# Kernel tuning notes

Hardware: AMD Instinct MI355X
Metric: run time of the kernel (lower is better)

Reference implementation:

```python
import jax, jax.numpy as jnp
import numpy as np


def setup_inputs() -> dict:
    key = jax.random.key(0)
    k1, k2, k3 = jax.random.split(key, 3)
    Lq, Lkv, H, D = 2048, 2048, 16, 128
    return {
        "query": jax.random.normal(k1, (Lq, H, D), dtype=jnp.float32),
        "key": jax.random.normal(k2, (Lkv, H, D), dtype=jnp.float32),
        "value": jax.random.normal(k3, (Lkv, H, D), dtype=jnp.float32),
    }


def reference(query, key, value):
    # query: [Lq, H, D], key: [Lkv, H, D], value: [Lkv, H, Dv]
    # Original module performs chunked online-softmax attention; the math is
    # exactly scaled-dot-product softmax attention with scale 1/sqrt(k_features).
    d = query.shape[-1]
    q = query * (1.0 / jnp.sqrt(jnp.asarray(d, dtype=query.dtype)))
    scores = jnp.einsum('qhd,khd->qhk', q, key)          # [Lq, H, Lkv]
    weights = jax.nn.softmax(scores, axis=-1)            # numerically stable online softmax equivalent
    out = jnp.einsum('qhk,khf->qhf', weights, value)     # [Lq, H, Dv]
    return out
```

## Files before the change

### kernel.cpp

```cpp
#include <hip/hip_runtime.h>
#include <hip/hip_bf16.h>

typedef __bf16 bf16x8 __attribute__((ext_vector_type(8)));
typedef __bf16 bf16x4 __attribute__((ext_vector_type(4)));
typedef __bf16 bf16x2 __attribute__((ext_vector_type(2)));
typedef float  f32x16 __attribute__((ext_vector_type(16)));
typedef float  f32x4  __attribute__((ext_vector_type(4)));

#define HD     2048
#define DH     128
#define KVT    64
#define NCH    16
#define NSPLIT 2
#define NROWS  32768
#define VSTR   68

__device__ __forceinline__ int kkey_of(int r) {
    return r & 7;
}

__global__ __launch_bounds__(512, 2)
void fmha_kern(const float* __restrict__ Qg, const float* __restrict__ Kg,
               const float* __restrict__ Vg, __bf16* __restrict__ wsOb,
               float* __restrict__ wsML)
{
    __shared__ __align__(16) __bf16 klds[2][KVT * 128];
    __shared__ __align__(16) __bf16 vtlds[2][DH * VSTR];

    const int tid  = threadIdx.x;
    const int lane = tid & 63;
    const int wrp  = tid >> 6;
    const int g    = lane >> 5;
    const int l31  = lane & 31;

    const int b    = blockIdx.x;
    const int grp  = b & 31;
    const int qblk = b >> 5;
    const int h    = grp >> 1;
    const int sp   = grp & 1;
    const int t0   = sp * NCH;

    const float qscale = 1.4426950408889634f * 0.08838834764831845f;
    const int q = qblk * 256 + wrp * 32 + l31;

    bf16x8 qf[8];
    {
        const float* qrow = Qg + (size_t)q * HD + h * DH;
        #pragma unroll
        for (int j = 0; j < 8; ++j) {
            f32x4 a = *(const f32x4*)(qrow + j * 16 + 8 * g);
            f32x4 c = *(const f32x4*)(qrow + j * 16 + 8 * g + 4);
            bf16x8 f;
            f[0] = (__bf16)(a[0] * qscale); f[1] = (__bf16)(a[1] * qscale);
            f[2] = (__bf16)(a[2] * qscale); f[3] = (__bf16)(a[3] * qscale);
            f[4] = (__bf16)(c[0] * qscale); f[5] = (__bf16)(c[1] * qscale);
            f[6] = (__bf16)(c[2] * qscale); f[7] = (__bf16)(c[3] * qscale);
            qf[j] = f;
        }
    }

    const int krow = tid >> 3, kc = tid & 7;
    const int kvp  = tid & 31, vdv0 = (tid >> 5) * 8;
    const float* kbase = Kg + (size_t)h * DH;
    const float* vbase = Vg + (size_t)h * DH;

    f32x4 kreg0, kreg1, kreg2, kreg3, vreg0, vreg1, vreg2, vreg3;

    auto stage_load = [&](int t) {
        const float* kp = kbase + (size_t)(t * KVT + krow) * HD + kc * 16;
        kreg0 = *(const f32x4*)(kp);
        kreg1 = *(const f32x4*)(kp + 4);
        kreg2 = *(const f32x4*)(kp + 8);
        kreg3 = *(const f32x4*)(kp + 12);
        const float* vp = vbase + (size_t)(t * KVT + 2 * kvp) * HD + vdv0;
        vreg0 = *(const f32x4*)(vp);
        vreg1 = *(const f32x4*)(vp + 4);
        vreg2 = *(const f32x4*)(vp + HD);
        vreg3 = *(const f32x4*)(vp + HD + 4);
    };

    auto stage_write = [&](int buf) {
        bf16x8 k0, k1;
        k0[0]=(__bf16)kreg0[0]; k0[1]=(__bf16)kreg0[1]; k0[2]=(__bf16)kreg0[2]; k0[3]=(__bf16)kreg0[3];
        k0[4]=(__bf16)kreg1[0]; k0[5]=(__bf16)kreg1[1]; k0[6]=(__bf16)kreg1[2]; k0[7]=(__bf16)kreg1[3];
        k1[0]=(__bf16)kreg2[0]; k1[1]=(__bf16)kreg2[1]; k1[2]=(__bf16)kreg2[2]; k1[3]=(__bf16)kreg2[3];
        k1[4]=(__bf16)kreg3[0]; k1[5]=(__bf16)kreg3[1]; k1[6]=(__bf16)kreg3[2]; k1[7]=(__bf16)kreg3[3];
        const int key = kkey_of(krow);
        *(bf16x8*)&klds[buf][krow * 128 + (((kc * 2)     ^ key) << 3)] = k0;
        *(bf16x8*)&klds[buf][krow * 128 + (((kc * 2 + 1) ^ key) << 3)] = k1;
        #pragma unroll
        for (int e = 0; e < 8; ++e) {
            bf16x2 w;
            w[0] = (__bf16)((e < 4) ? vreg0[e & 3] : vreg1[e & 3]);
            w[1] = (__bf16)((e < 4) ? vreg2[e & 3] : vreg3[e & 3]);
            *(bf16x2*)&vtlds[buf][(vdv0 + e) * VSTR + 2 * kvp] = w;
        }
    };

    auto block_sync = []() {
        asm volatile("s_waitcnt lgkmcnt(0)" ::: "memory");
        __builtin_amdgcn_s_barrier();
    };

    float mrun = -1e30f, lrun = 0.0f;
    f32x16 o0, o1, o2, o3;
    #pragma unroll
    for (int r = 0; r < 16; ++r) { o0[r] = 0.f; o1[r] = 0.f; o2[r] = 0.f; o3[r] = 0.f; }

    stage_load(t0);
    stage_write(0);
    stage_load(t0 + 1);
    block_sync();

    const int kkey = kkey_of(l31);

    #pragma unroll 2
    for (int tt = 0; tt < NCH; ++tt) {
        const int cur = tt & 1;

        f32x16 s0, s1;
        #pragma unroll
        for (int r = 0; r < 16; ++r) { s0[r] = 0.f; s1[r] = 0.f; }
        __builtin_amdgcn_s_setprio(1);
        #pragma unroll
        for (int j = 0; j < 8; ++j) {
            const int gcol = ((2 * j + g) ^ kkey) << 3;
            bf16x8 kf0 = *(const bf16x8*)&klds[cur][l31 * 128 + gcol];
            s0 = __builtin_amdgcn_mfma_f32_32x32x16_bf16(kf0, qf[j], s0, 0, 0, 0);
            bf16x8 kf1 = *(const bf16x8*)&klds[cur][(32 + l31) * 128 + gcol];
            s1 = __builtin_amdgcn_mfma_f32_32x32x16_bf16(kf1, qf[j], s1, 0, 0, 0);
        }
        __builtin_amdgcn_s_setprio(0);

        if (tt + 1 < NCH) stage_write(cur ^ 1);
        if (tt + 2 < NCH) stage_load(t0 + tt + 2);

        float m16[8];
        #pragma unroll
        for (int r = 0; r < 8; ++r)
            m16[r] = fmaxf(fmaxf(s0[r], s0[r + 8]), fmaxf(s1[r], s1[r + 8]));
        float tmax = fmaxf(fmaxf(fmaxf(m16[0], m16[4]), fmaxf(m16[1], m16[5])),
                           fmaxf(fmaxf(m16[2], m16[6]), fmaxf(m16[3], m16[7])));
        tmax = fmaxf(tmax, __shfl_xor(tmax, 32, 64));

        if (__any(tmax > mrun + 8.0f)) {
            const float mnew  = fmaxf(mrun, tmax);
            const float alpha = __builtin_amdgcn_exp2f(mrun - mnew);
            lrun *= alpha;
            #pragma unroll
            for (int r = 0; r < 16; ++r) { o0[r]*=alpha; o1[r]*=alpha; o2[r]*=alpha; o3[r]*=alpha; }
            mrun = mnew;
        }

        #pragma unroll
        for (int r = 0; r < 16; ++r) {
            s0[r] = __builtin_amdgcn_exp2f(s0[r] - mrun);
            s1[r] = __builtin_amdgcn_exp2f(s1[r] - mrun);
        }
        float ps = 0.f;
        #pragma unroll
        for (int r = 0; r < 16; ++r) ps += s0[r] + s1[r];
        lrun += ps;

        bf16x8 pfa0, pfa1, pfb0, pfb1;
        #pragma unroll
        for (int e = 0; e < 8; ++e) {
            pfa0[e] = (__bf16)s0[e]; pfa1[e] = (__bf16)s0[8 + e];
            pfb0[e] = (__bf16)s1[e]; pfb1[e] = (__bf16)s1[8 + e];
        }

        __builtin_amdgcn_s_setprio(1);
        #pragma unroll
        for (int bb = 0; bb < 4; ++bb) {
            const __bf16* vb = &vtlds[cur][(bb * 32 + l31) * VSTR];
            f32x16& oo = (bb == 0) ? o0 : (bb == 1) ? o1 : (bb == 2) ? o2 : o3;
            bf16x8 va;
            bf16x4 a0, a1;
            a0 = *(const bf16x4*)(vb + 4 * g);
            a1 = *(const bf16x4*)(vb + 8 + 4 * g);
            va[0]=a0[0]; va[1]=a0[1]; va[2]=a0[2]; va[3]=a0[3];
            va[4]=a1[0]; va[5]=a1[1]; va[6]=a1[2]; va[7]=a1[3];
            oo = __builtin_amdgcn_mfma_f32_32x32x16_bf16(va, pfa0, oo, 0, 0, 0);
            a0 = *(const bf16x4*)(vb + 16 + 4 * g);
            a1 = *(const bf16x4*)(vb + 24 + 4 * g);
            va[0]=a0[0]; va[1]=a0[1]; va[2]=a0[2]; va[3]=a0[3];
            va[4]=a1[0]; va[5]=a1[1]; va[6]=a1[2]; va[7]=a1[3];
            oo = __builtin_amdgcn_mfma_f32_32x32x16_bf16(va, pfa1, oo, 0, 0, 0);
            a0 = *(const bf16x4*)(vb + 32 + 4 * g);
            a1 = *(const bf16x4*)(vb + 40 + 4 * g);
            va[0]=a0[0]; va[1]=a0[1]; va[2]=a0[2]; va[3]=a0[3];
            va[4]=a1[0]; va[5]=a1[1]; va[6]=a1[2]; va[7]=a1[3];
            oo = __builtin_amdgcn_mfma_f32_32x32x16_bf16(va, pfb0, oo, 0, 0, 0);
            a0 = *(const bf16x4*)(vb + 48 + 4 * g);
            a1 = *(const bf16x4*)(vb + 56 + 4 * g);
            va[0]=a0[0]; va[1]=a0[1]; va[2]=a0[2]; va[3]=a0[3];
            va[4]=a1[0]; va[5]=a1[1]; va[6]=a1[2]; va[7]=a1[3];
            oo = __builtin_amdgcn_mfma_f32_32x32x16_bf16(va, pfb1, oo, 0, 0, 0);
        }
        __builtin_amdgcn_s_setprio(0);

        if (tt + 1 < NCH) block_sync();
    }

    const float ltot  = lrun + __shfl_xor(lrun, 32, 64);
    const int   rowid = q * 16 + h;

    __bf16* orow = wsOb + ((size_t)sp * NROWS + rowid) * 128;
    #pragma unroll
    for (int bb = 0; bb < 4; ++bb) {
        const f32x16& oo = (bb == 0) ? o0 : (bb == 1) ? o1 : (bb == 2) ? o2 : o3;
        #pragma unroll
        for (int jj = 0; jj < 4; ++jj) {
            bf16x4 v;
            v[0] = (__bf16)oo[4*jj+0]; v[1] = (__bf16)oo[4*jj+1];
            v[2] = (__bf16)oo[4*jj+2]; v[3] = (__bf16)oo[4*jj+3];
            *(bf16x4*)(orow + bb * 32 + 8 * jj + 4 * g) = v;
        }
    }
    if (lane < 32) {
        float* ml = wsML + ((size_t)sp * NROWS + rowid) * 2;
        ml[0] = mrun;
        ml[1] = ltot;
    }
}

__global__ __launch_bounds__(256, 4)
void fmha_combine(const __bf16* __restrict__ wsOb, const float* __restrict__ wsML,
                  float* __restrict__ Og)
{
    const int tid   = threadIdx.x;
    const int rowid = blockIdx.x * 8 + (tid >> 5);
    const int c     = (tid & 31) * 4;

    float m[NSPLIT], l[NSPLIT];
    float M = -1e30f;
    #pragma unroll
    for (int s = 0; s < NSPLIT; ++s) {
        const float* ml = wsML + ((size_t)s * NROWS + rowid) * 2;
        m[s] = ml[0]; l[s] = ml[1];
        M = fmaxf(M, m[s]);
    }
    float L = 0.f, w[NSPLIT];
    #pragma unroll
    for (int s = 0; s < NSPLIT; ++s) {
        w[s] = __builtin_amdgcn_exp2f(m[s] - M);
        L += l[s] * w[s];
    }
    const float inv = 1.0f / L;

    f32x4 acc; acc[0]=0.f; acc[1]=0.f; acc[2]=0.f; acc[3]=0.f;
    #pragma unroll
    for (int s = 0; s < NSPLIT; ++s) {
        bf16x4 v = *(const bf16x4*)(wsOb + ((size_t)s * NROWS + rowid) * 128 + c);
        acc[0] += (float)v[0] * w[s]; acc[1] += (float)v[1] * w[s];
        acc[2] += (float)v[2] * w[s]; acc[3] += (float)v[3] * w[s];
    }
    f32x4 r;
    r[0] = acc[0]*inv; r[1] = acc[1]*inv; r[2] = acc[2]*inv; r[3] = acc[3]*inv;
    *(f32x4*)(Og + (size_t)rowid * 128 + c) = r;
}

__global__ __launch_bounds__(256, 2)
void fmha_fb(const float* __restrict__ Qg, const float* __restrict__ Kg,
             const float* __restrict__ Vg, float* __restrict__ Og)
{
    __shared__ __align__(16) __bf16 klds[2][32 * 128];
    __shared__ __align__(16) __bf16 vtlds[2][DH * 36];

    const int tid  = threadIdx.x;
    const int lane = tid & 63;
    const int wrp  = tid >> 6;
    const int g    = lane >> 5;
    const int l31  = lane & 31;

    const int b    = blockIdx.x;
    const int h    = 2 * (b & 7) + ((b >> 3) >> 4);
    const int qblk = (b >> 3) & 15;

    const float qscale = 1.4426950408889634f * 0.08838834764831845f;
    const int q = qblk * 128 + wrp * 32 + l31;

    bf16x8 qf[8];
    {
        const float* qrow = Qg + (size_t)q * HD + h * DH;
        #pragma unroll
        for (int db = 0; db < 8; ++db) {
            f32x4 a = *(const f32x4*)(qrow + db * 16 + 8 * g);
            f32x4 c = *(const f32x4*)(qrow + db * 16 + 8 * g + 4);
            bf16x8 f;
            f[0] = (__bf16)(a[0] * qscale); f[1] = (__bf16)(a[1] * qscale);
            f[2] = (__bf16)(a[2] * qscale); f[3] = (__bf16)(a[3] * qscale);
            f[4] = (__bf16)(c[0] * qscale); f[5] = (__bf16)(c[1] * qscale);
            f[6] = (__bf16)(c[2] * qscale); f[7] = (__bf16)(c[3] * qscale);
            qf[db] = f;
        }
    }

    const int krow = tid >> 3, kc = tid & 7;
    const int vkv  = tid & 31, vdv0 = (tid >> 5) * 16;
    const float* kbase = Kg + (size_t)h * DH;
    const float* vbase = Vg + (size_t)h * DH;

    f32x4 kreg0, kreg1, kreg2, kreg3, vreg0, vreg1, vreg2, vreg3;

    auto stage_load = [&](int t) {
        const float* kp = kbase + (size_t)(t * 32 + krow) * HD + kc * 8;
        kreg0 = *(const f32x4*)(kp);
        kreg1 = *(const f32x4*)(kp + 4);
        kreg2 = *(const f32x4*)(kp + 64);
        kreg3 = *(const f32x4*)(kp + 68);
        const float* vp = vbase + (size_t)(t * 32 + vkv) * HD + vdv0;
        vreg0 = *(const f32x4*)(vp);
        vreg1 = *(const f32x4*)(vp + 4);
        vreg2 = *(const f32x4*)(vp + 8);
        vreg3 = *(const f32x4*)(vp + 12);
    };

    auto stage_write = [&](int buf) {
        bf16x8 k0, k1;
        k0[0]=(__bf16)kreg0[0]; k0[1]=(__bf16)kreg0[1]; k0[2]=(__bf16)kreg0[2]; k0[3]=(__bf16)kreg0[3];
        k0[4]=(__bf16)kreg1[0]; k0[5]=(__bf16)kreg1[1]; k0[6]=(__bf16)kreg1[2]; k0[7]=(__bf16)kreg1[3];
        k1[0]=(__bf16)kreg2[0]; k1[1]=(__bf16)kreg2[1]; k1[2]=(__bf16)kreg2[2]; k1[3]=(__bf16)kreg2[3];
        k1[4]=(__bf16)kreg3[0]; k1[5]=(__bf16)kreg3[1]; k1[6]=(__bf16)kreg3[2]; k1[7]=(__bf16)kreg3[3];
        const int swz = (krow & 7) << 3;
        *(bf16x8*)&klds[buf][krow * 128 + ((kc * 8) ^ swz)]      = k0;
        *(bf16x8*)&klds[buf][krow * 128 + ((kc * 8 + 64) ^ swz)] = k1;
        #pragma unroll
        for (int jj = 0; jj < 4; ++jj) {
            f32x4 vv = (jj == 0) ? vreg0 : (jj == 1) ? vreg1 : (jj == 2) ? vreg2 : vreg3;
            #pragma unroll
            for (int e = 0; e < 4; ++e)
                vtlds[buf][(vdv0 + jj * 4 + e) * 36 + vkv] = (__bf16)vv[e];
        }
    };

    float mrun = -1e30f, lrun = 0.0f;
    f32x16 o0, o1, o2, o3;
    #pragma unroll
    for (int r = 0; r < 16; ++r) { o0[r] = 0.f; o1[r] = 0.f; o2[r] = 0.f; o3[r] = 0.f; }

    stage_load(0);
    stage_write(0);

    for (int tt = 0; tt < 64; ++tt) {
        const int cur = tt & 1;
        if (tt + 1 < 64) stage_load(tt + 1);
        __syncthreads();

        f32x16 sa, sb;
        #pragma unroll
        for (int r = 0; r < 16; ++r) { sa[r] = 0.f; sb[r] = 0.f; }
        const int kswz = (l31 & 7) << 3;
        #pragma unroll
        for (int db = 0; db < 4; ++db) {
            bf16x8 kfa = *(const bf16x8*)&klds[cur][l31 * 128 + (((2*db)   * 16 + g * 8) ^ kswz)];
            sa = __builtin_amdgcn_mfma_f32_32x32x16_bf16(kfa, qf[2*db],   sa, 0, 0, 0);
            bf16x8 kfb = *(const bf16x8*)&klds[cur][l31 * 128 + (((2*db+1) * 16 + g * 8) ^ kswz)];
            sb = __builtin_amdgcn_mfma_f32_32x32x16_bf16(kfb, qf[2*db+1], sb, 0, 0, 0);
        }
        f32x16 s;
        #pragma unroll
        for (int r = 0; r < 16; ++r) s[r] = sa[r] + sb[r];

        float m8[8];
        #pragma unroll
        for (int r = 0; r < 8; ++r) m8[r] = fmaxf(s[r], s[r + 8]);
        float tmax = fmaxf(fmaxf(fmaxf(m8[0], m8[4]), fmaxf(m8[1], m8[5])),
                           fmaxf(fmaxf(m8[2], m8[6]), fmaxf(m8[3], m8[7])));
        tmax = fmaxf(tmax, __shfl_xor(tmax, 32, 64));

        if (__any(tmax > mrun + 8.0f)) {
            const float mnew  = fmaxf(mrun, tmax);
            const float alpha = __builtin_amdgcn_exp2f(mrun - mnew);
            lrun *= alpha;
            #pragma unroll
            for (int r = 0; r < 16; ++r) { o0[r] *= alpha; o1[r] *= alpha; o2[r] *= alpha; o3[r] *= alpha; }
            mrun = mnew;
        }

        float p[16];
        #pragma unroll
        for (int r = 0; r < 16; ++r) p[r] = __builtin_amdgcn_exp2f(s[r] - mrun);
        float ps0 = 0, ps1 = 0, ps2 = 0, ps3 = 0;
        #pragma unroll
        for (int r = 0; r < 4; ++r) { ps0 += p[r]; ps1 += p[r+4]; ps2 += p[r+8]; ps3 += p[r+12]; }
        lrun += ((ps0 + ps1) + (ps2 + ps3));

        bf16x8 pf0, pf1;
        #pragma unroll
        for (int e = 0; e < 8; ++e) { pf0[e] = (__bf16)p[e]; pf1[e] = (__bf16)p[8 + e]; }

        #pragma unroll
        for (int bb = 0; bb < 4; ++bb) {
            const __bf16* vb = &vtlds[cur][(bb * 32 + l31) * 36];
            bf16x4 a0 = *(const bf16x4*)(vb + 4 * g);
            bf16x4 a1 = *(const bf16x4*)(vb + 8 + 4 * g);
            bf16x8 va;
            va[0]=a0[0]; va[1]=a0[1]; va[2]=a0[2]; va[3]=a0[3];
            va[4]=a1[0]; va[5]=a1[1]; va[6]=a1[2]; va[7]=a1[3];
            f32x16& oo = (bb == 0) ? o0 : (bb == 1) ? o1 : (bb == 2) ? o2 : o3;
            oo = __builtin_amdgcn_mfma_f32_32x32x16_bf16(va, pf0, oo, 0, 0, 0);
            bf16x4 b0 = *(const bf16x4*)(vb + 16 + 4 * g);
            bf16x4 b1 = *(const bf16x4*)(vb + 24 + 4 * g);
            va[0]=b0[0]; va[1]=b0[1]; va[2]=b0[2]; va[3]=b0[3];
            va[4]=b1[0]; va[5]=b1[1]; va[6]=b1[2]; va[7]=b1[3];
            oo = __builtin_amdgcn_mfma_f32_32x32x16_bf16(va, pf1, oo, 0, 0, 0);
        }

        if (tt + 1 < 64) stage_write(cur ^ 1);
    }

    const float ltot = lrun + __shfl_xor(lrun, 32, 64);
    const float inv  = 1.0f / ltot;
    float* orow = Og + ((size_t)q * 16 + h) * 128;
    #pragma unroll
    for (int bb = 0; bb < 4; ++bb) {
        const f32x16& oo = (bb == 0) ? o0 : (bb == 1) ? o1 : (bb == 2) ? o2 : o3;
        #pragma unroll
        for (int jj = 0; jj < 4; ++jj) {
            f32x4 v;
            v[0] = oo[4*jj+0] * inv; v[1] = oo[4*jj+1] * inv;
            v[2] = oo[4*jj+2] * inv; v[3] = oo[4*jj+3] * inv;
            *(f32x4*)(orow + bb * 32 + 8 * jj + 4 * g) = v;
        }
    }
}

extern "C" void kernel_launch(void* const* d_in, const int* in_sizes, int n_in,
                              void* d_out, int out_size, void* d_ws, size_t ws_size,
                              hipStream_t stream) {
    const float* Q = (const float*)d_in[0];
    const float* K = (const float*)d_in[1];
    const float* V = (const float*)d_in[2];
    float* O = (float*)d_out;

    const size_t wsOb_b = (size_t)NSPLIT * NROWS * 128 * 2;
    const size_t wsML_b = (size_t)NSPLIT * NROWS * 2 * 4;
    const size_t need_bytes = wsOb_b + wsML_b;

    if (ws_size >= need_bytes) {
        __bf16* wsOb = (__bf16*)d_ws;
        float*  wsML = (float*)((char*)d_ws + wsOb_b);
        hipLaunchKernelGGL(fmha_kern, dim3(256), dim3(512), 0, stream,
                           Q, K, V, wsOb, wsML);
        hipLaunchKernelGGL(fmha_combine, dim3(NROWS / 8), dim3(256), 0, stream,
                           wsOb, wsML, O);
    } else {
        hipLaunchKernelGGL(fmha_fb, dim3(256), dim3(256), 0, stream, Q, K, V, O);
    }
}
```

Measured before the change: 65.36 us.

## Triple-buffer K/V tiles and overlap next QK^T with current softmax-PV

Grows the K and V^T shared-memory staging from two buffers to three and restructures the main loop into a software pipeline. The QK^T MFMAs for the next tile are issued before the softmax and PV of the current tile, using two sets of score registers. The aim is to hide softmax and exp latency behind matrix work. In exchange it uses about 1.5x the LDS, which may no longer fit two 512-thread blocks per CU, and needs more score registers under the 2-block launch bound, which raises spill risk.

```diff
diff --git a/kernel.cpp b/kernel.cpp
--- a/kernel.cpp
+++ b/kernel.cpp
@@ -15,17 +15,15 @@
 #define NROWS  32768
 #define VSTR   68
 
-__device__ __forceinline__ int kkey_of(int r) {
-    return r & 7;
-}
+__device__ __forceinline__ int kkey_of(int r) { return r & 7; }
 
 __global__ __launch_bounds__(512, 2)
 void fmha_kern(const float* __restrict__ Qg, const float* __restrict__ Kg,
                const float* __restrict__ Vg, __bf16* __restrict__ wsOb,
                float* __restrict__ wsML)
 {
-    __shared__ __align__(16) __bf16 klds[2][KVT * 128];
-    __shared__ __align__(16) __bf16 vtlds[2][DH * VSTR];
+    __shared__ __align__(16) __bf16 klds[3][KVT * 128];
+    __shared__ __align__(16) __bf16 vtlds[3][DH * VSTR];
 
     const int tid  = threadIdx.x;
     const int lane = tid & 63;
@@ -107,34 +105,24 @@
     #pragma unroll
     for (int r = 0; r < 16; ++r) { o0[r] = 0.f; o1[r] = 0.f; o2[r] = 0.f; o3[r] = 0.f; }
 
-    stage_load(t0);
-    stage_write(0);
-    stage_load(t0 + 1);
-    block_sync();
-
     const int kkey = kkey_of(l31);
 
-    #pragma unroll 2
-    for (int tt = 0; tt < NCH; ++tt) {
-        const int cur = tt & 1;
-
-        f32x16 s0, s1;
-        #pragma unroll
-        for (int r = 0; r < 16; ++r) { s0[r] = 0.f; s1[r] = 0.f; }
+    auto qk = [&](int buf, f32x16& r0, f32x16& r1) {
+        #pragma unroll
+        for (int r = 0; r < 16; ++r) { r0[r] = 0.f; r1[r] = 0.f; }
         __builtin_amdgcn_s_setprio(1);
         #pragma unroll
         for (int j = 0; j < 8; ++j) {
             const int gcol = ((2 * j + g) ^ kkey) << 3;
-            bf16x8 kf0 = *(const bf16x8*)&klds[cur][l31 * 128 + gcol];
-            s0 = __builtin_amdgcn_mfma_f32_32x32x16_bf16(kf0, qf[j], s0, 0, 0, 0);
-            bf16x8 kf1 = *(const bf16x8*)&klds[cur][(32 + l31) * 128 + gcol];
-            s1 = __builtin_amdgcn_mfma_f32_32x32x16_bf16(kf1, qf[j], s1, 0, 0, 0);
+            bf16x8 kf0 = *(const bf16x8*)&klds[buf][l31 * 128 + gcol];
+            r0 = __builtin_amdgcn_mfma_f32_32x32x16_bf16(kf0, qf[j], r0, 0, 0, 0);
+            bf16x8 kf1 = *(const bf16x8*)&klds[buf][(32 + l31) * 128 + gcol];
+            r1 = __builtin_amdgcn_mfma_f32_32x32x16_bf16(kf1, qf[j], r1, 0, 0, 0);
         }
         __builtin_amdgcn_s_setprio(0);
-
-        if (tt + 1 < NCH) stage_write(cur ^ 1);
-        if (tt + 2 < NCH) stage_load(t0 + tt + 2);
-
+    };
+
+    auto softmax_pv = [&](f32x16& s0, f32x16& s1, int buf) {
         float m16[8];
         #pragma unroll
         for (int r = 0; r < 8; ++r)
@@ -172,7 +160,7 @@
         __builtin_amdgcn_s_setprio(1);
         #pragma unroll
         for (int bb = 0; bb < 4; ++bb) {
-            const __bf16* vb = &vtlds[cur][(bb * 32 + l31) * VSTR];
+            const __bf16* vb = &vtlds[buf][(bb * 32 + l31) * VSTR];
             f32x16& oo = (bb == 0) ? o0 : (bb == 1) ? o1 : (bb == 2) ? o2 : o3;
             bf16x8 va;
             bf16x4 a0, a1;
@@ -198,8 +186,30 @@
             oo = __builtin_amdgcn_mfma_f32_32x32x16_bf16(va, pfb1, oo, 0, 0, 0);
         }
         __builtin_amdgcn_s_setprio(0);
-
-        if (tt + 1 < NCH) block_sync();
+    };
+
+    stage_load(t0);     stage_write(0);
+    stage_load(t0 + 1); stage_write(1);
+    stage_load(t0 + 2);
+    block_sync();
+
+    f32x16 sA0, sA1, sB0, sB1;
+    qk(0, sA0, sA1);
+
+    #pragma unroll 1
+    for (int tt = 0; tt < NCH; tt += 2) {
+        qk((tt + 1) % 3, sB0, sB1);
+        if (tt + 2 < NCH) stage_write((tt + 2) % 3);
+        if (tt + 3 < NCH) stage_load(t0 + tt + 3);
+        softmax_pv(sA0, sA1, tt % 3);
+        block_sync();
+        if (tt + 2 < NCH) {
+            qk((tt + 2) % 3, sA0, sA1);
+            if (tt + 3 < NCH) stage_write((tt + 3) % 3);
+            if (tt + 4 < NCH) stage_load(t0 + tt + 4);
+        }
+        softmax_pv(sB0, sB1, (tt + 1) % 3);
+        if (tt + 2 < NCH) block_sync();
     }
 
     const float ltot  = lrun + __shfl_xor(lrun, 32, 64);
```

Measured after the change: 72.34 us. 1.11x slower.
